# Kernel optimization log

Hardware: AMD Instinct MI355X
Metric: run time of the kernel (lower is better)

The kernel has to match this reference:

```python
import jax, jax.numpy as jnp
import numpy as np

E = 1024      # embed_dim
H = 16        # num_heads
HD = E // H   # head_dim = 64
WIN = 256     # window_size
LN_EPS = 1e-5


def _layernorm(x, g, b):
    mu = jnp.mean(x, axis=-1, keepdims=True)
    var = jnp.var(x, axis=-1, keepdims=True)
    return (x - mu) * jax.lax.rsqrt(var + LN_EPS) * g + b


def _rope_tables(S):
    freqs = 1.0 / (10000.0 ** (jnp.arange(0, HD, 2, dtype=jnp.float32) / HD))  # [HD/2]
    t = jnp.arange(S, dtype=jnp.float32)
    fr = jnp.outer(t, freqs)                      # [S, HD/2]
    emb = jnp.concatenate([fr, fr], axis=-1)      # [S, HD]
    # shape [S, 1, HD] so it broadcasts over the heads dim of [B, S, H, HD]
    return emb[:, None, :].astype(jnp.float32), None


def _rotate_half(x):
    x1, x2 = jnp.split(x, 2, axis=-1)
    return jnp.concatenate([-x2, x1], axis=-1)


def setup_inputs() -> dict:
    key = jax.random.key(0)
    ks = jax.random.split(key, 12)
    B, S = 8, 1024
    sc = 0.02
    return {
        "x": jax.random.normal(ks[0], (B, S, E), dtype=jnp.float32),
        "in_proj_w": jax.random.normal(ks[1], (3 * E, E), dtype=jnp.float32) * sc,
        "in_proj_b": jnp.zeros((3 * E,), dtype=jnp.float32),
        "out_proj_w": jax.random.normal(ks[2], (E, E), dtype=jnp.float32) * sc,
        "out_proj_b": jnp.zeros((E,), dtype=jnp.float32),
        "ln1_g": jnp.ones((E,), dtype=jnp.float32),
        "ln1_b": jnp.zeros((E,), dtype=jnp.float32),
        "w1": jax.random.normal(ks[3], (4 * E, E), dtype=jnp.float32) * sc,
        "b1": jnp.zeros((4 * E,), dtype=jnp.float32),
        "w2": jax.random.normal(ks[4], (E, 4 * E), dtype=jnp.float32) * sc,
        "b2": jnp.zeros((E,), dtype=jnp.float32),
        "ln2_g": jnp.ones((E,), dtype=jnp.float32),
        "ln2_b": jnp.zeros((E,), dtype=jnp.float32),
    }


def reference(x, in_proj_w, in_proj_b, out_proj_w, out_proj_b,
              ln1_g, ln1_b, w1, b1, w2, b2, ln2_g, ln2_b):
    B, S, _ = x.shape
    # RoPE applied to the raw input (pre in_proj), as in the torch module
    emb, _ = _rope_tables(S)
    cos, sin = jnp.cos(emb), jnp.sin(emb)          # [S, 1, HD]
    xh = x.reshape(B, S, H, HD)
    roped = xh * cos + _rotate_half(xh) * sin      # [B, S, H, HD]
    qk_in = roped.reshape(B, S, E)

    Wq, Wk, Wv = jnp.split(in_proj_w, 3, axis=0)   # each [E, E]
    bq, bk, bv = jnp.split(in_proj_b, 3, axis=0)
    q = (qk_in @ Wq.T + bq).reshape(B, S, H, HD).transpose(0, 2, 1, 3)  # [B,H,S,HD]
    k = (qk_in @ Wk.T + bk).reshape(B, S, H, HD).transpose(0, 2, 1, 3)
    v = (x @ Wv.T + bv).reshape(B, S, H, HD).transpose(0, 2, 1, 3)

    scale = 1.0 / np.sqrt(HD)
    scores = jnp.einsum("bhqd,bhkd->bhqk", q, k) * scale  # [B,H,S,S]
    idx = jnp.arange(S)
    disallowed = jnp.abs(idx[:, None] - idx[None, :]) > WIN  # [S,S] bool
    scores = jnp.where(disallowed, jnp.float32(-jnp.inf), scores)
    attn = jax.nn.softmax(scores, axis=-1)
    ctx = jnp.einsum("bhqk,bhkd->bhqd", attn, v)            # [B,H,S,HD]
    ctx = ctx.transpose(0, 2, 1, 3).reshape(B, S, E)
    h = ctx @ out_proj_w.T + out_proj_b

    x1 = _layernorm(x + h, ln1_g, ln1_b)
    ff = jax.nn.gelu(x1 @ w1.T + b1, approximate=False) @ w2.T + b2
    return _layernorm(x1 + ff, ln2_g, ln2_b)
```

## Files before the change

### kernel.cpp

```cpp
#include <hip/hip_runtime.h>
#include <stdint.h>


#define B_ 8
#define S_ 1024
#define E_ 1024
#define H_ 16
#define HD_ 64
#define WIN_ 256
#define QKV_ 3072

typedef __attribute__((ext_vector_type(8))) short short8;
typedef __attribute__((ext_vector_type(4))) float f32x4;
typedef __attribute__((ext_vector_type(4))) unsigned short us4;
typedef unsigned short ushort_t;

__device__ __forceinline__ ushort_t f2b(float f) {
  unsigned int u = __builtin_bit_cast(unsigned int, f);
  u = (u + 0x7fffu + ((u >> 16) & 1u)) >> 16;
  return (ushort_t)u;
}

__device__ __forceinline__ ushort_t f2b_trunc(float f) {
  return (ushort_t)(__builtin_bit_cast(unsigned int, f) >> 16);
}

__device__ __forceinline__ float b2f(ushort_t u) {
  return __builtin_bit_cast(float, ((unsigned int)u) << 16);
}

__device__ __forceinline__ float fast_exp2(float x) {
#if __has_builtin(__builtin_amdgcn_exp2f)
  return __builtin_amdgcn_exp2f(x);
#else
  return exp2f(x);
#endif
}

__device__ __forceinline__ float fast_rcp(float x) {
#if __has_builtin(__builtin_amdgcn_rcpf)
  return __builtin_amdgcn_rcpf(x);
#else
  return 1.f / x;
#endif
}

__device__ __forceinline__ void gld_lds16(const void* g, void* l) {
  __builtin_amdgcn_global_load_lds((const __attribute__((address_space(1))) void*)g,
                                   (__attribute__((address_space(3))) void*)l, 16, 0, 0);
}

__global__ __launch_bounds__(256) void cast4_kernel(const float* __restrict__ i0,
                                                    const float* __restrict__ i1,
                                                    const float* __restrict__ i2,
                                                    const float* __restrict__ i3,
                                                    ushort_t* __restrict__ o0,
                                                    ushort_t* __restrict__ o1,
                                                    ushort_t* __restrict__ o2,
                                                    ushort_t* __restrict__ o3) {
  int i = blockIdx.x * 256 + threadIdx.x;
  const float* in;
  ushort_t* out;
  int j;
  if (i < 786432)       { in = i0; out = o0; j = i; }
  else if (i < 1048576) { in = i1; out = o1; j = i - 786432; }
  else if (i < 2097152) { in = i2; out = o2; j = i - 1048576; }
  else                  { in = i3; out = o3; j = i - 2097152; }
  float4 v = ((const float4*)in)[j];
  us4 o;
  o.x = f2b(v.x); o.y = f2b(v.y); o.z = f2b(v.z); o.w = f2b(v.w);
  ((us4*)out)[j] = o;
}

__global__ __launch_bounds__(256) void rope_kernel(const float* __restrict__ x,
                                                   ushort_t* __restrict__ roped,
                                                   ushort_t* __restrict__ xbf) {
  int idx = blockIdx.x * 256 + threadIdx.x;
  int d = idx & 31;
  int h = (idx >> 5) & 15;
  int s = (idx >> 9) & 1023;
  int b = idx >> 19;
  size_t base = ((size_t)(b * S_ + s)) * E_ + h * HD_ + d;
  float x0 = x[base], x1 = x[base + 32];
  float freq = exp2f(-(float)d * 0.41524101186092029f);
  float th = (float)s * freq;
  float sn, cs;
  sincosf(th, &sn, &cs);
  roped[base]      = f2b(x0 * cs - x1 * sn);
  roped[base + 32] = f2b(x1 * cs + x0 * sn);
  xbf[base]      = f2b(x0);
  xbf[base + 32] = f2b(x1);
}

template <int MODE>
__global__ __launch_bounds__(256) void gemm_bt(const ushort_t* __restrict__ A,
                                               const ushort_t* __restrict__ A2,
                                               int nsplit,
                                               const ushort_t* __restrict__ Bm,
                                               const float* __restrict__ bias,
                                               ushort_t* __restrict__ C,
                                               int N, int K) {
  __shared__ ushort_t sA[128 * 64];
  __shared__ ushort_t sB[128 * 64];
  const int tid = threadIdx.x;
  const int lane = tid & 63;
  const int wave = tid >> 6;
  const int quad = lane >> 4;
  const int lq = lane & 15;
  const int wm = (wave & 1) * 64;
  const int wn = (wave >> 1) * 64;
  const size_t bm = (size_t)blockIdx.x * 128;
  const size_t bn = (size_t)blockIdx.y * 128;
  const ushort_t* Asel = (bn >= (size_t)nsplit) ? A2 : A;

  f32x4 acc[4][4] = {};

  const int srow = lane >> 3;
  const int skc = ((lane & 7) ^ (lane >> 3)) * 8;

  for (int k0 = 0; k0 < K; k0 += 64) {
#pragma unroll
    for (int i = 0; i < 4; i++) {
      const int r0 = wave * 32 + i * 8;
      gld_lds16(Asel + (bm + r0 + srow) * K + k0 + skc, &sA[r0 * 64]);
      gld_lds16(Bm + (bn + r0 + srow) * K + k0 + skc, &sB[r0 * 64]);
    }
    __syncthreads();

#pragma unroll
    for (int kk = 0; kk < 2; kk++) {
      const int csw = (((kk * 4) + quad) ^ (lq & 7)) * 8;
      short8 av[4], bv[4];
#pragma unroll
      for (int mt = 0; mt < 4; mt++)
        av[mt] = *(const short8*)&sA[(wm + mt * 16 + lq) * 64 + csw];
#pragma unroll
      for (int nt = 0; nt < 4; nt++)
        bv[nt] = *(const short8*)&sB[(wn + nt * 16 + lq) * 64 + csw];
#pragma unroll
      for (int mt = 0; mt < 4; mt++)
#pragma unroll
        for (int nt = 0; nt < 4; nt++)
          acc[mt][nt] = __builtin_amdgcn_mfma_f32_16x16x32_bf16(av[mt], bv[nt], acc[mt][nt], 0, 0, 0);
    }
    __syncthreads();
  }

#pragma unroll
  for (int mt = 0; mt < 4; mt++) {
#pragma unroll
    for (int nt = 0; nt < 4; nt++) {
      size_t row = bm + wm + mt * 16 + quad * 4;
      size_t col = bn + wn + nt * 16 + lq;
      float bc = bias[col];
#pragma unroll
      for (int r = 0; r < 4; r++) {
        float v = acc[mt][nt][r] + bc;
        if (MODE == 1) {
          float y = 0.7978845608028654f * (v + 0.044715f * v * v * v);
          float t = fast_exp2(y * 2.8853900817779268f);
          v = v * (t * fast_rcp(1.f + t));
        }
        C[(row + r) * N + col] = f2b(v);
      }
    }
  }
}

#define FENCE asm volatile("" ::: "memory")
#define VM6 asm volatile("s_waitcnt vmcnt(6)" ::: "memory")
#define VM0 asm volatile("s_waitcnt vmcnt(0)" ::: "memory")
#define NOPW ((void)0)

#define STAGE_A(bufc, half, kb)                                               \
  { gld_lds16(aSrc + (size_t)((half) * 128) * K + (kb),                       \
              &lds[16384 * (bufc) + 8192 * (half) + wave * 512]);             \
    gld_lds16(aSrc + (size_t)((half) * 128 + 64) * K + (kb),                  \
              &lds[16384 * (bufc) + 8192 * (half) + 4096 + wave * 512]); }

#define STAGE_B(bufc, half, kb)                                               \
  { gld_lds16(bSrc + (size_t)((half) * 128) * K + (kb),                       \
              &lds[32768 + 16384 * (bufc) + 8192 * (half) + wave * 512]);     \
    gld_lds16(bSrc + (size_t)((half) * 128 + 64) * K + (kb),                  \
              &lds[32768 + 16384 * (bufc) + 8192 * (half) + 4096 + wave * 512]); }

#define PHASE(qq, bufc, doA, doB, STAGE_STMT, WAIT_STMT)                      \
  {                                                                           \
    if (doA) {                                                                \
      const int abase = 16384 * (bufc) + 8192 * ((qq) >> 1);                  \
      _Pragma("unroll") for (int mf = 0; mf < 4; mf++) {                      \
        const int ra = wm * 64 + mf * 16 + lq;                                \
        _Pragma("unroll") for (int k2 = 0; k2 < 2; k2++)                      \
          av[mf][k2] = *(const short8*)&lds[abase + ra * 64 +                 \
                                            (((k2 * 4 + quad) ^ (lq & 7)) << 3)]; \
      }                                                                       \
    }                                                                         \
    if (doB) {                                                                \
      const int bbase = 32768 + 16384 * (bufc) +                              \
                        8192 * ((((qq) == 1) || ((qq) == 2)) ? 1 : 0);        \
      _Pragma("unroll") for (int nf = 0; nf < 2; nf++) {                      \
        const int rb = wn * 32 + nf * 16 + lq;                                \
        _Pragma("unroll") for (int k2 = 0; k2 < 2; k2++)                      \
          bv[nf][k2] = *(const short8*)&lds[bbase + rb * 64 +                 \
                                            (((k2 * 4 + quad) ^ (lq & 7)) << 3)]; \
      }                                                                       \
    }                                                                         \
    STAGE_STMT;                                                               \
    FENCE; __builtin_amdgcn_s_barrier(); FENCE;                               \
    __builtin_amdgcn_s_setprio(1);                                            \
    _Pragma("unroll") for (int k2 = 0; k2 < 2; k2++)                          \
      _Pragma("unroll") for (int mf = 0; mf < 4; mf++)                        \
        _Pragma("unroll") for (int nf = 0; nf < 2; nf++)                      \
          acc[qq][mf][nf] = __builtin_amdgcn_mfma_f32_16x16x32_bf16(          \
              av[mf][k2], bv[nf][k2], acc[qq][mf][nf], 0, 0, 0);              \
    __builtin_amdgcn_s_setprio(0);                                            \
    WAIT_STMT;                                                                \
    FENCE; __builtin_amdgcn_s_barrier(); FENCE;                               \
  }

template <int MODE>
__global__ __launch_bounds__(512, 2) void gemm256(const ushort_t* __restrict__ A,
                                                  const ushort_t* __restrict__ A2,
                                                  int nsplit,
                                                  const ushort_t* __restrict__ Bm,
                                                  const float* __restrict__ bias,
                                                  ushort_t* __restrict__ C,
                                                  int N, int Klen, int K,
                                                  int nbx, int nbn,
                                                  int CX, int CY) {
  __shared__ ushort_t lds[65536];
  const int tid = threadIdx.x;
  const int lane = tid & 63, wave = tid >> 6;
  const int quad = lane >> 4, lq = lane & 15;
  const int wm = wave >> 2, wn = wave & 3;

  const int nwg = gridDim.x;
  const int id = blockIdx.x;
  int bx, byt;
  if (nwg & 7) {
    bx = id % nbx; byt = id / nbx;
  } else {
    const int within = id >> 3;
    const int chunk = id & 7;
    const int nchx = nbx / CX;
    bx = (chunk % nchx) * CX + (within % CX);
    byt = (chunk / nchx) * CY + (within / CX);
  }
  const int bny = byt % nbn;
  const int ks = byt / nbn;
  const size_t bm = (size_t)bx * 256, bn = (size_t)bny * 256;
  const ushort_t* Asel = ((int)bn >= nsplit) ? A2 : A;
  const size_t koff = (size_t)ks * Klen;

  const int srow = lane >> 3;
  const int scol = ((lane & 7) ^ srow) << 3;
  const ushort_t* aSrc = Asel + (bm + wave * 8 + srow) * (size_t)K + koff + scol;
  const ushort_t* bSrc = Bm + (bn + wave * 8 + srow) * (size_t)K + koff + scol;

  f32x4 acc[4][4][2] = {};
  short8 av[4][2], bv[2][2];

  STAGE_A(0, 0, 0); STAGE_A(0, 1, 0); STAGE_B(0, 0, 0); STAGE_B(0, 1, 0);
  STAGE_A(1, 0, 64); STAGE_B(1, 1, 64); STAGE_A(1, 1, 64);
  VM6;
  FENCE; __builtin_amdgcn_s_barrier(); FENCE;

  const int NT = Klen >> 6;
#pragma unroll 1
  for (int i = 0; i < (NT >> 1) - 1; i++) {
    const int kb0 = i << 7;
    PHASE(0, 0, 1, 1, STAGE_B(1, 0, kb0 + 64), NOPW);
    PHASE(1, 0, 0, 1, STAGE_A(0, 0, kb0 + 128), NOPW);
    PHASE(2, 0, 1, 0, STAGE_B(0, 1, kb0 + 128), NOPW);
    PHASE(3, 0, 0, 1, STAGE_A(0, 1, kb0 + 128), VM6);
    PHASE(0, 1, 1, 1, STAGE_B(0, 0, kb0 + 128), NOPW);
    PHASE(1, 1, 0, 1, STAGE_A(1, 0, kb0 + 192), NOPW);
    PHASE(2, 1, 1, 0, STAGE_B(1, 1, kb0 + 192), NOPW);
    PHASE(3, 1, 0, 1, STAGE_A(1, 1, kb0 + 192), VM6);
  }
  {
    const int kb0 = (NT - 2) << 6;
    PHASE(0, 0, 1, 1, STAGE_B(1, 0, kb0 + 64), NOPW);
    PHASE(1, 0, 0, 1, NOPW, NOPW);
    PHASE(2, 0, 1, 0, NOPW, NOPW);
    PHASE(3, 0, 0, 1, NOPW, VM0);
    PHASE(0, 1, 1, 1, NOPW, NOPW);
    PHASE(1, 1, 0, 1, NOPW, NOPW);
    PHASE(2, 1, 1, 0, NOPW, NOPW);
    PHASE(3, 1, 0, 1, NOPW, NOPW);
  }

  float* Pf = (MODE == 2) ? (ks ? (float*)bias : (float*)C) : nullptr;
#pragma unroll
  for (int q = 0; q < 4; q++) {
    const int Mh = q >> 1;
    const int Nh = (q == 1 || q == 2) ? 1 : 0;
#pragma unroll
    for (int mf = 0; mf < 4; mf++) {
#pragma unroll
      for (int nf = 0; nf < 2; nf++) {
        size_t row = bm + Mh * 128 + wm * 64 + mf * 16 + quad * 4;
        size_t col = bn + Nh * 128 + wn * 32 + nf * 16 + lq;
        float bc = (MODE == 2) ? 0.f : bias[col];
#pragma unroll
        for (int r = 0; r < 4; r++) {
          float v = acc[q][mf][nf][r] + bc;
          if (MODE == 1) {
            float y = 0.7978845608028654f * (v + 0.044715f * v * v * v);
            float t = fast_exp2(y * 2.8853900817779268f);
            v = v * (t * fast_rcp(1.f + t));
          }
          if (MODE == 2) {
            Pf[(row + r) * (size_t)N + col] = v;
          } else {
            C[(row + r) * N + col] = f2b(v);
          }
        }
      }
    }
  }
}

__global__ __launch_bounds__(256) void vtrans_kernel(const ushort_t* __restrict__ qkv,
                                                     ushort_t* __restrict__ vt) {
  __shared__ ushort_t tb[64 * 65];
  int bh = blockIdx.x >> 4;
  int st = blockIdx.x & 15;
  int b = bh >> 4, h = bh & 15;
  int s0 = st * 64;
  int tid = threadIdx.x;
  int c = tid & 63, rbase = tid >> 6;
#pragma unroll
  for (int rep = 0; rep < 16; rep++) {
    int i = rep * 4 + rbase;
    tb[c * 65 + i] = qkv[(size_t)(b * S_ + s0 + i) * QKV_ + 2048 + h * HD_ + c];
  }
  __syncthreads();
#pragma unroll
  for (int rep = 0; rep < 16; rep++) {
    int d = rep * 4 + rbase;
    vt[(size_t)((b * H_ + h) * HD_ + d) * S_ + s0 + c] = tb[d * 65 + c];
  }
}

#define SC_ 0.18033688011112042f

__global__ __launch_bounds__(256) void attn_kernel(const ushort_t* __restrict__ qkv,
                                                   const ushort_t* __restrict__ vt,
                                                   ushort_t* __restrict__ ctx) {
  __shared__ ushort_t sK[2][32 * 64];
  __shared__ ushort_t sV[2][64 * 32];
  __shared__ ushort_t sP[4][16 * 36];
  const int tid = threadIdx.x;
  const int lane = tid & 63, wave = tid >> 6;
  const int quad = lane >> 4, lq = lane & 15;
  int gid = ((blockIdx.x & 7) << 8) | (blockIdx.x >> 3);
  int qs = gid & 15;
  int h = (gid >> 4) & 15;
  int b = gid >> 8;
  int qs64 = qs * 64;
  int q0 = qs64 + wave * 16;

  const size_t qoff = (size_t)(b * S_ + q0 + lq) * QKV_ + h * HD_;
  short8 a0 = *(const short8*)&qkv[qoff + quad * 8];
  short8 a1 = *(const short8*)&qkv[qoff + 32 + quad * 8];

  f32x4 o[4] = {};
  float rs[4] = {0.f, 0.f, 0.f, 0.f};

  int start = qs64 - WIN_; if (start < 0) start = 0;
  int end = qs64 + 64 + WIN_; if (end > S_) end = S_;
  const int wlo = q0 - WIN_;
  const int whi = q0 + 16 + WIN_;

  const ushort_t* kg = qkv + (size_t)(b * S_) * QKV_ + 1024 + h * HD_;
  const ushort_t* vg = vt + (size_t)((b * H_ + h) * HD_) * S_;

  const int krow = lane >> 3;
  const int kchg = ((lane & 7) ^ krow) << 3;
  const int vrow = lane >> 2;
  const int vchg = ((lane & 3) ^ ((lane >> 3) & 3)) << 3;

  gld_lds16(kg + (size_t)(start + wave * 8 + krow) * QKV_ + kchg, &sK[0][wave * 512]);
  gld_lds16(vg + (size_t)(wave * 16 + vrow) * S_ + start + vchg, &sV[0][wave * 512]);

  const int nch = (end - start) >> 5;
  int buf = 0;
  for (int c = 0; c < nch; c++) {
    __syncthreads();
    int kb = start + c * 32;
    if (c + 1 < nch) {
      int nkb = kb + 32;
      gld_lds16(kg + (size_t)(nkb + wave * 8 + krow) * QKV_ + kchg, &sK[buf ^ 1][wave * 512]);
      gld_lds16(vg + (size_t)(wave * 16 + vrow) * S_ + nkb + vchg, &sV[buf ^ 1][wave * 512]);
    }
    if (kb < whi && kb + 32 > wlo) {
      f32x4 s[2];
#pragma unroll
      for (int t = 0; t < 2; t++) {
        const ushort_t* kr = &sK[buf][(t * 16 + lq) * 64];
        short8 b0 = *(const short8*)&kr[((quad ^ (lq & 7)) << 3)];
        short8 b1 = *(const short8*)&kr[(((4 + quad) ^ (lq & 7)) << 3)];
        f32x4 z = {};
        z = __builtin_amdgcn_mfma_f32_16x16x32_bf16(a0, b0, z, 0, 0, 0);
        z = __builtin_amdgcn_mfma_f32_16x16x32_bf16(a1, b1, z, 0, 0, 0);
        s[t] = z;
      }
      float p[2][4];
      const bool full = (kb >= q0 - 241) && (kb <= q0 + 225);
      if (full) {
#pragma unroll
        for (int t = 0; t < 2; t++)
#pragma unroll
          for (int r = 0; r < 4; r++) p[t][r] = fast_exp2(s[t][r] * SC_);
      } else {
#pragma unroll
        for (int t = 0; t < 2; t++) {
          int ki = kb + t * 16 + lq;
#pragma unroll
          for (int r = 0; r < 4; r++) {
            int dd = q0 + quad * 4 + r - ki;
            bool allowed = (dd <= WIN_) && (dd >= -WIN_);
            p[t][r] = allowed ? fast_exp2(s[t][r] * SC_) : 0.f;
          }
        }
      }
#pragma unroll
      for (int r = 0; r < 4; r++) rs[r] += p[0][r] + p[1][r];

#pragma unroll
      for (int t = 0; t < 2; t++)
#pragma unroll
        for (int r = 0; r < 4; r++)
          sP[wave][(quad * 4 + r) * 36 + t * 16 + lq] = f2b_trunc(p[t][r]);
      asm volatile("s_waitcnt lgkmcnt(0)" ::: "memory");
      short8 ap = *(const short8*)&sP[wave][lq * 36 + quad * 8];

#pragma unroll
      for (int nt = 0; nt < 4; nt++) {
        short8 bvf = *(const short8*)&sV[buf][(nt * 16 + lq) * 32 +
                                             ((quad ^ ((lq >> 1) & 3)) << 3)];
        o[nt] = __builtin_amdgcn_mfma_f32_16x16x32_bf16(ap, bvf, o[nt], 0, 0, 0);
      }
    }
    buf ^= 1;
  }

  float inv[4];
#pragma unroll
  for (int r = 0; r < 4; r++) {
    float v = rs[r];
    v += __shfl_xor(v, 1);
    v += __shfl_xor(v, 2);
    v += __shfl_xor(v, 4);
    v += __shfl_xor(v, 8);
    inv[r] = 1.f / v;
  }

#pragma unroll
  for (int nt = 0; nt < 4; nt++)
#pragma unroll
    for (int r = 0; r < 4; r++) {
      int row = q0 + quad * 4 + r;
      int col = h * HD_ + nt * 16 + lq;
      ctx[(size_t)(b * S_ + row) * E_ + col] = f2b(o[nt][r] * inv[r]);
    }
}

__global__ __launch_bounds__(256) void ln_res_kernel(const float* __restrict__ A,
                                                     const ushort_t* __restrict__ Bv,
                                                     const float* __restrict__ g,
                                                     const float* __restrict__ be,
                                                     float* __restrict__ outf,
                                                     ushort_t* __restrict__ outb) {
  const int row = blockIdx.x;
  const int tid = threadIdx.x;
  const size_t base = (size_t)row * 1024;
  float4 a4 = ((const float4*)(A + base))[tid];
  us4 b4 = ((const us4*)(Bv + base))[tid];
  float v[4];
  v[0] = a4.x + b2f(b4.x);
  v[1] = a4.y + b2f(b4.y);
  v[2] = a4.z + b2f(b4.z);
  v[3] = a4.w + b2f(b4.w);
  float s = v[0] + v[1] + v[2] + v[3];
  float sq = v[0] * v[0] + v[1] * v[1] + v[2] * v[2] + v[3] * v[3];
#pragma unroll
  for (int off = 32; off; off >>= 1) {
    s += __shfl_xor(s, off);
    sq += __shfl_xor(sq, off);
  }
  __shared__ float ls[4], lsq[4];
  int wave = tid >> 6, lane = tid & 63;
  if (lane == 0) { ls[wave] = s; lsq[wave] = sq; }
  __syncthreads();
  s = ls[0] + ls[1] + ls[2] + ls[3];
  sq = lsq[0] + lsq[1] + lsq[2] + lsq[3];
  float mean = s * (1.f / 1024.f);
  float var = sq * (1.f / 1024.f) - mean * mean;
  float rstd = rsqrtf(var + 1e-5f);
  float4 g4 = ((const float4*)g)[tid];
  float4 e4 = ((const float4*)be)[tid];
  float o0 = (v[0] - mean) * rstd * g4.x + e4.x;
  float o1 = (v[1] - mean) * rstd * g4.y + e4.y;
  float o2 = (v[2] - mean) * rstd * g4.z + e4.z;
  float o3 = (v[3] - mean) * rstd * g4.w + e4.w;
  float4 of = {o0, o1, o2, o3};
  ((float4*)(outf + base))[tid] = of;
  if (outb) {
    us4 ob;
    ob.x = f2b(o0); ob.y = f2b(o1); ob.z = f2b(o2); ob.w = f2b(o3);
    ((us4*)(outb + base))[tid] = ob;
  }
}

__global__ __launch_bounds__(256) void ln_res2_kernel(const float* __restrict__ A,
                                                      const float* __restrict__ P0,
                                                      const float* __restrict__ P1,
                                                      const float* __restrict__ bias,
                                                      const float* __restrict__ g,
                                                      const float* __restrict__ be,
                                                      float* __restrict__ outf) {
  const int row = blockIdx.x;
  const int tid = threadIdx.x;
  const size_t base = (size_t)row * 1024;
  float4 a4 = ((const float4*)(A + base))[tid];
  float4 p04 = ((const float4*)(P0 + base))[tid];
  float4 p14 = ((const float4*)(P1 + base))[tid];
  float4 bi4 = ((const float4*)bias)[tid];
  float v[4];
  v[0] = a4.x + p04.x + p14.x + bi4.x;
  v[1] = a4.y + p04.y + p14.y + bi4.y;
  v[2] = a4.z + p04.z + p14.z + bi4.z;
  v[3] = a4.w + p04.w + p14.w + bi4.w;
  float s = v[0] + v[1] + v[2] + v[3];
  float sq = v[0] * v[0] + v[1] * v[1] + v[2] * v[2] + v[3] * v[3];
#pragma unroll
  for (int off = 32; off; off >>= 1) {
    s += __shfl_xor(s, off);
    sq += __shfl_xor(sq, off);
  }
  __shared__ float ls[4], lsq[4];
  int wave = tid >> 6, lane = tid & 63;
  if (lane == 0) { ls[wave] = s; lsq[wave] = sq; }
  __syncthreads();
  s = ls[0] + ls[1] + ls[2] + ls[3];
  sq = lsq[0] + lsq[1] + lsq[2] + lsq[3];
  float mean = s * (1.f / 1024.f);
  float var = sq * (1.f / 1024.f) - mean * mean;
  float rstd = rsqrtf(var + 1e-5f);
  float4 g4 = ((const float4*)g)[tid];
  float4 e4 = ((const float4*)be)[tid];
  float4 of;
  of.x = (v[0] - mean) * rstd * g4.x + e4.x;
  of.y = (v[1] - mean) * rstd * g4.y + e4.y;
  of.z = (v[2] - mean) * rstd * g4.z + e4.z;
  of.w = (v[3] - mean) * rstd * g4.w + e4.w;
  ((float4*)(outf + base))[tid] = of;
}

#define O_XBF   ((size_t)0)
#define O_ROPED ((size_t)16777216)
#define O_W_IN  ((size_t)33554432)
#define O_W_OUT ((size_t)39845888)
#define O_W1    ((size_t)41943040)
#define O_W2    ((size_t)50331648)
#define O_BIG   ((size_t)58720256)
#define O_VT    ((size_t)125829120)
#define O_X1F   ((size_t)142606336)
#define O_P1    ((size_t)176160768)

extern "C" void kernel_launch(void* const* d_in, const int* in_sizes, int n_in,
                              void* d_out, int out_size, void* d_ws, size_t ws_size,
                              hipStream_t stream) {
  const float* x          = (const float*)d_in[0];
  const float* in_proj_w  = (const float*)d_in[1];
  const float* in_proj_b  = (const float*)d_in[2];
  const float* out_proj_w = (const float*)d_in[3];
  const float* out_proj_b = (const float*)d_in[4];
  const float* ln1_g      = (const float*)d_in[5];
  const float* ln1_b      = (const float*)d_in[6];
  const float* w1         = (const float*)d_in[7];
  const float* b1         = (const float*)d_in[8];
  const float* w2         = (const float*)d_in[9];
  const float* b2         = (const float*)d_in[10];
  const float* ln2_g      = (const float*)d_in[11];
  const float* ln2_b      = (const float*)d_in[12];
  float* out = (float*)d_out;

  char* ws = (char*)d_ws;
  ushort_t* xbf     = (ushort_t*)(ws + O_XBF);
  ushort_t* roped   = (ushort_t*)(ws + O_ROPED);
  ushort_t* wbf_in  = (ushort_t*)(ws + O_W_IN);
  ushort_t* wbf_out = (ushort_t*)(ws + O_W_OUT);
  ushort_t* wbf_1   = (ushort_t*)(ws + O_W1);
  ushort_t* wbf_2   = (ushort_t*)(ws + O_W2);
  ushort_t* qkv_buf = (ushort_t*)(ws + O_BIG);
  ushort_t* vtb     = (ushort_t*)(ws + O_VT);
  ushort_t* ctx     = (ushort_t*)(ws + O_ROPED);
  ushort_t* h_bf    = (ushort_t*)(ws + O_BIG);
  float*    x1f     = (float*)(ws + O_X1F);
  ushort_t* x1bf    = (ushort_t*)(ws + O_XBF);
  ushort_t* ff1     = (ushort_t*)(ws + O_BIG);
  float*    p0      = (float*)(ws + O_XBF);
  float*    p1      = (float*)(ws + O_P1);

  dim3 blk(256);
  dim3 blk512(512);
  const int NOSPLIT = 1 << 30;

  cast4_kernel<<<dim3(12288), blk, 0, stream>>>(in_proj_w, out_proj_w, w1, w2,
                                                wbf_in, wbf_out, wbf_1, wbf_2);

  rope_kernel<<<dim3(16384), blk, 0, stream>>>(x, roped, xbf);

  gemm256<0><<<dim3(384), blk512, 0, stream>>>(roped, xbf, 2048, wbf_in, in_proj_b,
                                               qkv_buf, QKV_, 1024, 1024, 32, 12, 8, 6);
  vtrans_kernel<<<dim3(2048), blk, 0, stream>>>(qkv_buf, vtb);

  attn_kernel<<<dim3(2048), blk, 0, stream>>>(qkv_buf, vtb, ctx);

  gemm_bt<0><<<dim3(64, 8), blk, 0, stream>>>(ctx, ctx, NOSPLIT, wbf_out, out_proj_b,
                                              h_bf, 1024, 1024);

  ln_res_kernel<<<dim3(8192), blk, 0, stream>>>(x, h_bf, ln1_g, ln1_b, x1f, x1bf);

  gemm256<1><<<dim3(512), blk512, 0, stream>>>(x1bf, x1bf, NOSPLIT, wbf_1, b1,
                                               ff1, 4096, 1024, 1024, 32, 16, 8, 8);

  gemm256<2><<<dim3(256), blk512, 0, stream>>>(ff1, ff1, NOSPLIT, wbf_2,
                                               (const float*)p1, (ushort_t*)p0,
                                               1024, 2048, 4096, 32, 4, 8, 4);

  ln_res2_kernel<<<dim3(8192), blk, 0, stream>>>(x1f, p0, p1, b2, ln2_g, ln2_b, out);
}
```

Before: 442.4 us.

## Load GEMM A operand directly from global into registers, stage only B in LDS

Restructures the 256x256 GEMM main loop so the A tile is no longer staged through LDS. Each wave instead reads its A fragments straight from global memory into double-buffered registers (av0/av1). Only B is staged in LDS, which halves shared memory per block and removes the A LDS reads and writes. The cost is uncoalesced, latency-exposed global loads for A, which are duplicated across the four waves sharing a row block, plus higher register pressure. The waitcnt scheme is also changed, with only a prologue wait remaining, which risks data hazards on the B buffers.

```diff
diff --git a/kernel.cpp b/kernel.cpp
--- a/kernel.cpp
+++ b/kernel.cpp
@@ -168,42 +168,30 @@
 }
 
 #define FENCE asm volatile("" ::: "memory")
-#define VM6 asm volatile("s_waitcnt vmcnt(6)" ::: "memory")
-#define VM0 asm volatile("s_waitcnt vmcnt(0)" ::: "memory")
+#define VM12 asm volatile("s_waitcnt vmcnt(12)" ::: "memory")
 #define NOPW ((void)0)
-
-#define STAGE_A(bufc, half, kb)                                               \
-  { gld_lds16(aSrc + (size_t)((half) * 128) * K + (kb),                       \
-              &lds[16384 * (bufc) + 8192 * (half) + wave * 512]);             \
-    gld_lds16(aSrc + (size_t)((half) * 128 + 64) * K + (kb),                  \
-              &lds[16384 * (bufc) + 8192 * (half) + 4096 + wave * 512]); }
 
 #define STAGE_B(bufc, half, kb)                                               \
   { gld_lds16(bSrc + (size_t)((half) * 128) * K + (kb),                       \
-              &lds[32768 + 16384 * (bufc) + 8192 * (half) + wave * 512]);     \
+              &lds[16384 * (bufc) + 8192 * (half) + wave * 512]);             \
     gld_lds16(bSrc + (size_t)((half) * 128 + 64) * K + (kb),                  \
-              &lds[32768 + 16384 * (bufc) + 8192 * (half) + 4096 + wave * 512]); }
-
-#define PHASE(qq, bufc, doA, doB, STAGE_STMT, WAIT_STMT)                      \
+              &lds[16384 * (bufc) + 8192 * (half) + 4096 + wave * 512]); }
+
+#define AV_LOAD(dst, Mh, kt)                                                  \
+  _Pragma("unroll") for (int mf = 0; mf < 4; mf++)                            \
+    _Pragma("unroll") for (int k2 = 0; k2 < 2; k2++)                          \
+      dst[mf][k2] = *(const short8*)(aRow +                                   \
+          (size_t)((Mh) * 128 + mf * 16) * K + (kt) + k2 * 32);
+
+#define PHASE2(qq, bufc, DOREADS, STAGE_STMT, AV_STMT)                        \
   {                                                                           \
-    if (doA) {                                                                \
-      const int abase = 16384 * (bufc) + 8192 * ((qq) >> 1);                  \
-      _Pragma("unroll") for (int mf = 0; mf < 4; mf++) {                      \
-        const int ra = wm * 64 + mf * 16 + lq;                                \
-        _Pragma("unroll") for (int k2 = 0; k2 < 2; k2++)                      \
-          av[mf][k2] = *(const short8*)&lds[abase + ra * 64 +                 \
-                                            (((k2 * 4 + quad) ^ (lq & 7)) << 3)]; \
-      }                                                                       \
-    }                                                                         \
-    if (doB) {                                                                \
-      const int bbase = 32768 + 16384 * (bufc) +                              \
-                        8192 * ((((qq) == 1) || ((qq) == 2)) ? 1 : 0);        \
-      _Pragma("unroll") for (int nf = 0; nf < 2; nf++) {                      \
-        const int rb = wn * 32 + nf * 16 + lq;                                \
-        _Pragma("unroll") for (int k2 = 0; k2 < 2; k2++)                      \
-          bv[nf][k2] = *(const short8*)&lds[bbase + rb * 64 +                 \
-                                            (((k2 * 4 + quad) ^ (lq & 7)) << 3)]; \
-      }                                                                       \
+    if (DOREADS) {                                                            \
+      _Pragma("unroll") for (int nh = 0; nh < 2; nh++)                        \
+        _Pragma("unroll") for (int nf = 0; nf < 2; nf++)                      \
+          _Pragma("unroll") for (int k2 = 0; k2 < 2; k2++)                    \
+            bvv[nh][nf][k2] = *(const short8*)&lds[16384 * (bufc) +           \
+                8192 * nh + (wn * 32 + nf * 16 + lq) * 64 +                   \
+                (((k2 * 4 + quad) ^ (lq & 7)) << 3)];                         \
     }                                                                         \
     STAGE_STMT;                                                               \
     FENCE; __builtin_amdgcn_s_barrier(); FENCE;                               \
@@ -212,9 +200,11 @@
       _Pragma("unroll") for (int mf = 0; mf < 4; mf++)                        \
         _Pragma("unroll") for (int nf = 0; nf < 2; nf++)                      \
           acc[qq][mf][nf] = __builtin_amdgcn_mfma_f32_16x16x32_bf16(          \
-              av[mf][k2], bv[nf][k2], acc[qq][mf][nf], 0, 0, 0);              \
+              ((qq) < 2 ? av0 : av1)[mf][k2],                                 \
+              bvv[(((qq) == 1) || ((qq) == 2)) ? 1 : 0][nf][k2],              \
+              acc[qq][mf][nf], 0, 0, 0);                                      \
     __builtin_amdgcn_s_setprio(0);                                            \
-    WAIT_STMT;                                                                \
+    AV_STMT;                                                                  \
     FENCE; __builtin_amdgcn_s_barrier(); FENCE;                               \
   }
 
@@ -228,7 +218,7 @@
                                                   int N, int Klen, int K,
                                                   int nbx, int nbn,
                                                   int CX, int CY) {
-  __shared__ ushort_t lds[65536];
+  __shared__ ushort_t lds[32768];
   const int tid = threadIdx.x;
   const int lane = tid & 63, wave = tid >> 6;
   const int quad = lane >> 4, lq = lane & 15;
@@ -254,40 +244,43 @@
 
   const int srow = lane >> 3;
   const int scol = ((lane & 7) ^ srow) << 3;
-  const ushort_t* aSrc = Asel + (bm + wave * 8 + srow) * (size_t)K + koff + scol;
   const ushort_t* bSrc = Bm + (bn + wave * 8 + srow) * (size_t)K + koff + scol;
+  const ushort_t* aRow = Asel + (bm + wm * 64 + lq) * (size_t)K + koff + quad * 8;
 
   f32x4 acc[4][4][2] = {};
-  short8 av[4][2], bv[2][2];
-
-  STAGE_A(0, 0, 0); STAGE_A(0, 1, 0); STAGE_B(0, 0, 0); STAGE_B(0, 1, 0);
-  STAGE_A(1, 0, 64); STAGE_B(1, 1, 64); STAGE_A(1, 1, 64);
-  VM6;
+  short8 av0[4][2], av1[4][2], bvv[2][2][2];
+
+  STAGE_B(0, 0, 0); STAGE_B(0, 1, 0);
+  FENCE;
+  AV_LOAD(av0, 0, 0);
+  FENCE;
+  STAGE_B(1, 0, 64); STAGE_B(1, 1, 64);
+  VM12;
   FENCE; __builtin_amdgcn_s_barrier(); FENCE;
 
   const int NT = Klen >> 6;
 #pragma unroll 1
   for (int i = 0; i < (NT >> 1) - 1; i++) {
     const int kb0 = i << 7;
-    PHASE(0, 0, 1, 1, STAGE_B(1, 0, kb0 + 64), NOPW);
-    PHASE(1, 0, 0, 1, STAGE_A(0, 0, kb0 + 128), NOPW);
-    PHASE(2, 0, 1, 0, STAGE_B(0, 1, kb0 + 128), NOPW);
-    PHASE(3, 0, 0, 1, STAGE_A(0, 1, kb0 + 128), VM6);
-    PHASE(0, 1, 1, 1, STAGE_B(0, 0, kb0 + 128), NOPW);
-    PHASE(1, 1, 0, 1, STAGE_A(1, 0, kb0 + 192), NOPW);
-    PHASE(2, 1, 1, 0, STAGE_B(1, 1, kb0 + 192), NOPW);
-    PHASE(3, 1, 0, 1, STAGE_A(1, 1, kb0 + 192), VM6);
+    PHASE2(0, 0, 1, NOPW, AV_LOAD(av1, 1, kb0));
+    PHASE2(1, 0, 0, NOPW, AV_LOAD(av0, 0, kb0 + 64));
+    PHASE2(2, 0, 0, STAGE_B(0, 0, kb0 + 128), NOPW);
+    PHASE2(3, 0, 0, STAGE_B(0, 1, kb0 + 128), NOPW);
+    PHASE2(0, 1, 1, NOPW, AV_LOAD(av1, 1, kb0 + 64));
+    PHASE2(1, 1, 0, NOPW, AV_LOAD(av0, 0, kb0 + 128));
+    PHASE2(2, 1, 0, STAGE_B(1, 0, kb0 + 192), NOPW);
+    PHASE2(3, 1, 0, STAGE_B(1, 1, kb0 + 192), NOPW);
   }
   {
     const int kb0 = (NT - 2) << 6;
-    PHASE(0, 0, 1, 1, STAGE_B(1, 0, kb0 + 64), NOPW);
-    PHASE(1, 0, 0, 1, NOPW, NOPW);
-    PHASE(2, 0, 1, 0, NOPW, NOPW);
-    PHASE(3, 0, 0, 1, NOPW, VM0);
-    PHASE(0, 1, 1, 1, NOPW, NOPW);
-    PHASE(1, 1, 0, 1, NOPW, NOPW);
-    PHASE(2, 1, 1, 0, NOPW, NOPW);
-    PHASE(3, 1, 0, 1, NOPW, NOPW);
+    PHASE2(0, 0, 1, NOPW, AV_LOAD(av1, 1, kb0));
+    PHASE2(1, 0, 0, NOPW, AV_LOAD(av0, 0, kb0 + 64));
+    PHASE2(2, 0, 0, NOPW, NOPW);
+    PHASE2(3, 0, 0, NOPW, NOPW);
+    PHASE2(0, 1, 1, NOPW, AV_LOAD(av1, 1, kb0 + 64));
+    PHASE2(1, 1, 0, NOPW, NOPW);
+    PHASE2(2, 1, 0, NOPW, NOPW);
+    PHASE2(3, 1, 0, NOPW, NOPW);
   }
 
   float* Pf = (MODE == 2) ? (ks ? (float*)bias : (float*)C) : nullptr;
```

Result: slower. 860.0 us (+94.4%).

## Restructure gemm256 main loop into two-quadrant phases with interleaved LDS reads

Applied to the files above, without the earlier changes.

The 256x256 GEMM main loop is rescheduled from eight single-quadrant phases per iteration into four phases, each issuing two global-to-LDS stages and two MFMA quadrant blocks. A B-fragment LDS read is placed between the two quadrant blocks. This halves the number of barriers per K-step and overlaps LDS reads with MFMA work, and the vmcnt wait thresholds and prologue staging are adjusted to match. It risks changing how far ahead prefetch runs, and correctness depends on the new buffer reuse order staying race-free.

```diff
diff --git a/kernel.cpp b/kernel.cpp
--- a/kernel.cpp
+++ b/kernel.cpp
@@ -168,7 +168,7 @@
 }
 
 #define FENCE asm volatile("" ::: "memory")
-#define VM6 asm volatile("s_waitcnt vmcnt(6)" ::: "memory")
+#define VM4 asm volatile("s_waitcnt vmcnt(4)" ::: "memory")
 #define VM0 asm volatile("s_waitcnt vmcnt(0)" ::: "memory")
 #define NOPW ((void)0)
 
@@ -184,36 +184,47 @@
     gld_lds16(bSrc + (size_t)((half) * 128 + 64) * K + (kb),                  \
               &lds[32768 + 16384 * (bufc) + 8192 * (half) + 4096 + wave * 512]); }
 
-#define PHASE(qq, bufc, doA, doB, STAGE_STMT, WAIT_STMT)                      \
+#define READ_A(bufc, Mh)                                                      \
+  _Pragma("unroll") for (int mf = 0; mf < 4; mf++)                            \
+    _Pragma("unroll") for (int k2 = 0; k2 < 2; k2++)                          \
+      av[mf][k2] = *(const short8*)&lds[16384 * (bufc) + 8192 * (Mh) +        \
+          (wm * 64 + mf * 16 + lq) * 64 + (((k2 * 4 + quad) ^ (lq & 7)) << 3)];
+
+#define READ_B(bufc, half)                                                    \
+  _Pragma("unroll") for (int nf = 0; nf < 2; nf++)                            \
+    _Pragma("unroll") for (int k2 = 0; k2 < 2; k2++)                          \
+      bv[nf][k2] = *(const short8*)&lds[32768 + 16384 * (bufc) +              \
+          8192 * (half) + (wn * 32 + nf * 16 + lq) * 64 +                     \
+          (((k2 * 4 + quad) ^ (lq & 7)) << 3)];
+
+#define MFMA_Q(qq)                                                            \
+  __builtin_amdgcn_s_setprio(1);                                              \
+  _Pragma("unroll") for (int k2 = 0; k2 < 2; k2++)                            \
+    _Pragma("unroll") for (int mf = 0; mf < 4; mf++)                          \
+      _Pragma("unroll") for (int nf = 0; nf < 2; nf++)                        \
+        acc[qq][mf][nf] = __builtin_amdgcn_mfma_f32_16x16x32_bf16(            \
+            av[mf][k2], bv[nf][k2], acc[qq][mf][nf], 0, 0, 0);                \
+  __builtin_amdgcn_s_setprio(0);
+
+#define PHASE_A(bufc, S1, S2)                                                 \
   {                                                                           \
-    if (doA) {                                                                \
-      const int abase = 16384 * (bufc) + 8192 * ((qq) >> 1);                  \
-      _Pragma("unroll") for (int mf = 0; mf < 4; mf++) {                      \
-        const int ra = wm * 64 + mf * 16 + lq;                                \
-        _Pragma("unroll") for (int k2 = 0; k2 < 2; k2++)                      \
-          av[mf][k2] = *(const short8*)&lds[abase + ra * 64 +                 \
-                                            (((k2 * 4 + quad) ^ (lq & 7)) << 3)]; \
-      }                                                                       \
-    }                                                                         \
-    if (doB) {                                                                \
-      const int bbase = 32768 + 16384 * (bufc) +                              \
-                        8192 * ((((qq) == 1) || ((qq) == 2)) ? 1 : 0);        \
-      _Pragma("unroll") for (int nf = 0; nf < 2; nf++) {                      \
-        const int rb = wn * 32 + nf * 16 + lq;                                \
-        _Pragma("unroll") for (int k2 = 0; k2 < 2; k2++)                      \
-          bv[nf][k2] = *(const short8*)&lds[bbase + rb * 64 +                 \
-                                            (((k2 * 4 + quad) ^ (lq & 7)) << 3)]; \
-      }                                                                       \
-    }                                                                         \
-    STAGE_STMT;                                                               \
+    READ_A(bufc, 0); READ_B(bufc, 0);                                         \
+    S1; S2;                                                                   \
     FENCE; __builtin_amdgcn_s_barrier(); FENCE;                               \
-    __builtin_amdgcn_s_setprio(1);                                            \
-    _Pragma("unroll") for (int k2 = 0; k2 < 2; k2++)                          \
-      _Pragma("unroll") for (int mf = 0; mf < 4; mf++)                        \
-        _Pragma("unroll") for (int nf = 0; nf < 2; nf++)                      \
-          acc[qq][mf][nf] = __builtin_amdgcn_mfma_f32_16x16x32_bf16(          \
-              av[mf][k2], bv[nf][k2], acc[qq][mf][nf], 0, 0, 0);              \
-    __builtin_amdgcn_s_setprio(0);                                            \
+    MFMA_Q(0);                                                                \
+    READ_B(bufc, 1);                                                          \
+    MFMA_Q(1);                                                                \
+    FENCE; __builtin_amdgcn_s_barrier(); FENCE;                               \
+  }
+
+#define PHASE_B(bufc, S1, S2, WAIT_STMT)                                      \
+  {                                                                           \
+    READ_A(bufc, 1);                                                          \
+    S1; S2;                                                                   \
+    FENCE; __builtin_amdgcn_s_barrier(); FENCE;                               \
+    MFMA_Q(2);                            \
+    READ_B(bufc, 0);                                                          \
+    MFMA_Q(3);                                                                \
     WAIT_STMT;                                                                \
     FENCE; __builtin_amdgcn_s_barrier(); FENCE;                               \
   }
@@ -261,33 +272,25 @@
   short8 av[4][2], bv[2][2];
 
   STAGE_A(0, 0, 0); STAGE_A(0, 1, 0); STAGE_B(0, 0, 0); STAGE_B(0, 1, 0);
-  STAGE_A(1, 0, 64); STAGE_B(1, 1, 64); STAGE_A(1, 1, 64);
-  VM6;
+  STAGE_A(1, 0, 64); STAGE_B(1, 1, 64);
+  VM4;
   FENCE; __builtin_amdgcn_s_barrier(); FENCE;
 
   const int NT = Klen >> 6;
 #pragma unroll 1
   for (int i = 0; i < (NT >> 1) - 1; i++) {
     const int kb0 = i << 7;
-    PHASE(0, 0, 1, 1, STAGE_B(1, 0, kb0 + 64), NOPW);
-    PHASE(1, 0, 0, 1, STAGE_A(0, 0, kb0 + 128), NOPW);
-    PHASE(2, 0, 1, 0, STAGE_B(0, 1, kb0 + 128), NOPW);
-    PHASE(3, 0, 0, 1, STAGE_A(0, 1, kb0 + 128), VM6);
-    PHASE(0, 1, 1, 1, STAGE_B(0, 0, kb0 + 128), NOPW);
-    PHASE(1, 1, 0, 1, STAGE_A(1, 0, kb0 + 192), NOPW);
-    PHASE(2, 1, 1, 0, STAGE_B(1, 1, kb0 + 192), NOPW);
-    PHASE(3, 1, 0, 1, STAGE_A(1, 1, kb0 + 192), VM6);
+    PHASE_A(0, STAGE_B(1, 0, kb0 + 64),  STAGE_A(1, 1, kb0 + 64));
+    PHASE_B(0, STAGE_A(0, 0, kb0 + 128), STAGE_B(0, 1, kb0 + 128), VM4);
+    PHASE_A(1, STAGE_B(0, 0, kb0 + 128), STAGE_A(0, 1, kb0 + 128));
+    PHASE_B(1, STAGE_A(1, 0, kb0 + 192), STAGE_B(1, 1, kb0 + 192), VM4);
   }
   {
-    const int kb0 = (NT - 2) << 6;
-    PHASE(0, 0, 1, 1, STAGE_B(1, 0, kb0 + 64), NOPW);
-    PHASE(1, 0, 0, 1, NOPW, NOPW);
-    PHASE(2, 0, 1, 0, NOPW, NOPW);
-    PHASE(3, 0, 0, 1, NOPW, VM0);
-    PHASE(0, 1, 1, 1, NOPW, NOPW);
-    PHASE(1, 1, 0, 1, NOPW, NOPW);
-    PHASE(2, 1, 1, 0, NOPW, NOPW);
-    PHASE(3, 1, 0, 1, NOPW, NOPW);
+    const int kbL = (NT - 2) << 6;
+    PHASE_A(0, STAGE_B(1, 0, kbL + 64), STAGE_A(1, 1, kbL + 64));
+    PHASE_B(0, NOPW, NOPW, VM0);
+    PHASE_A(1, NOPW, NOPW);
+    PHASE_B(1, NOPW, NOPW, NOPW);
   }
 
   float* Pf = (MODE == 2) ? (ks ? (float*)bias : (float*)C) : nullptr;
```

Measured after the change: 456.8 us. +3.3%, slower.
